# Optimization experiments

Hardware: AMD Instinct MI355X
Metric: run time of the kernel (lower is better)

The kernel has to match this reference:

```python
import jax, jax.numpy as jnp
import numpy as np

# KernelNorm2d config (matches init_kwargs)
KH, KW = 2, 2          # kernel_size
SH, SW = 2, 2          # stride
PAD = (0, 0, 0, 0)     # (left, right, top, bottom) as in F.pad on last two dims
EPS = 1e-5

B, C, H, W = 16, 64, 256, 256


def setup_inputs() -> dict:
    key = jax.random.key(0)
    x = jax.random.normal(key, (B, C, H, W), dtype=jnp.float32)
    return {"x": x}


def _kernel_norm2d(x):
    left, right, top, bottom = PAD
    xp = jnp.pad(x, ((0, 0), (0, 0), (top, bottom), (left, right)))
    b, c, hp, wp = xp.shape
    nH = (hp - KH) // SH + 1
    nW = (wp - KW) // SW + 1
    # Gather window pixels: output pixel (i*KH+a, j*KW+b) <- padded (i*SH+a, j*SW+b).
    rows = (jnp.arange(nH)[:, None] * SH + jnp.arange(KH)[None, :]).reshape(-1)
    cols = (jnp.arange(nW)[:, None] * SW + jnp.arange(KW)[None, :]).reshape(-1)
    g = xp[:, :, rows, :][:, :, :, cols]              # [B, C, nH*KH, nW*KW]
    gr = g.reshape(b, c, nH, KH, nW, KW)
    # Per-window mean/var over (C, KH, KW); biased var (unbiased=False).
    mu = jnp.mean(gr, axis=(1, 3, 5), keepdims=True)  # [B,1,nH,1,nW,1]
    m2 = jnp.mean(gr * gr, axis=(1, 3, 5), keepdims=True)
    var = m2 - mu * mu
    out = (gr - mu) / jnp.sqrt(var + EPS)
    return out.reshape(b, c, nH * KH, nW * KW)


def reference(x):
    return _kernel_norm2d(x)
```

## Files before the change

kernel.cpp:

```cpp
#include <hip/hip_runtime.h>


#define CC 64
#define HH 256
#define WW 256

__global__ __launch_bounds__(256)
void knorm2d_kernel(const float* __restrict__ x, float* __restrict__ out) {
    const int t   = threadIdx.x;
    const int blk = blockIdx.x;
    const int b   = blk >> 9;
    const int rem = blk & 511;
    const int i   = rem >> 2;
    const int cc  = rem & 3;
    const int vq  = t & 15;

    const size_t base = (size_t)b * (CC * HH * WW) + (size_t)(2 * i) * WW
                      + (size_t)(64 * cc + 4 * vq);

    float4 data[8];
    float sum[2] = {0.f, 0.f};
    float ssq[2] = {0.f, 0.f};

    #pragma unroll
    for (int k = 0; k < 8; ++k) {
        const int idx = k * 256 + t;
        const int seg = idx >> 4;
        const int c   = seg >> 1;
        const int hoff= seg & 1;
        const size_t off = base + (size_t)c * (HH * WW) + (size_t)hoff * WW;
        const float4 v = *reinterpret_cast<const float4*>(x + off);
        data[k] = v;
        sum[0] += v.x + v.y;   ssq[0] += v.x * v.x + v.y * v.y;
        sum[1] += v.z + v.w;   ssq[1] += v.z * v.z + v.w * v.w;
    }

    #pragma unroll
    for (int q = 0; q < 2; ++q) {
        sum[q] += __shfl_xor(sum[q], 16);
        ssq[q] += __shfl_xor(ssq[q], 16);
        sum[q] += __shfl_xor(sum[q], 32);
        ssq[q] += __shfl_xor(ssq[q], 32);
    }

    __shared__ float part[4][16][4];
    __shared__ float stats[32][2];

    const int wave = t >> 6;
    const int lid  = t & 63;
    if (lid < 16) {
        part[wave][lid][0] = sum[0];
        part[wave][lid][1] = ssq[0];
        part[wave][lid][2] = sum[1];
        part[wave][lid][3] = ssq[1];
    }
    __syncthreads();

    if (t < 32) {
        const int v = t >> 1;
        const int q = t & 1;
        float s = 0.f, s2 = 0.f;
        #pragma unroll
        for (int w = 0; w < 4; ++w) {
            s  += part[w][v][2 * q];
            s2 += part[w][v][2 * q + 1];
        }
        const float mu  = s  * (1.0f / 256.0f);
        const float var = s2 * (1.0f / 256.0f) - mu * mu;
        stats[t][0] = mu;
        stats[t][1] = rsqrtf(var + 1e-5f);
    }
    __syncthreads();

    const float mu0 = stats[2 * vq][0],     rs0 = stats[2 * vq][1];
    const float mu1 = stats[2 * vq + 1][0], rs1 = stats[2 * vq + 1][1];

    #pragma unroll
    for (int k = 0; k < 8; ++k) {
        const int idx = k * 256 + t;
        const int seg = idx >> 4;
        const int c   = seg >> 1;
        const int hoff= seg & 1;
        const size_t off = base + (size_t)c * (HH * WW) + (size_t)hoff * WW;
        float4 v = data[k];
        float4 o;
        o.x = (v.x - mu0) * rs0;
        o.y = (v.y - mu0) * rs0;
        o.z = (v.z - mu1) * rs1;
        o.w = (v.w - mu1) * rs1;
        *reinterpret_cast<float4*>(out + off) = o;
    }
}

extern "C" void kernel_launch(void* const* d_in, const int* in_sizes, int n_in,
                              void* d_out, int out_size, void* d_ws, size_t ws_size,
                              hipStream_t stream) {
    const float* x = (const float*)d_in[0];
    float* out     = (float*)d_out;
    knorm2d_kernel<<<dim3(8192), dim3(256), 0, stream>>>(x, out);
}
```

Baseline: 436.6 us.

## Use 1024-thread blocks covering full row pairs with nontemporal output stores

```diff
diff --git a/kernel.cpp b/kernel.cpp
--- a/kernel.cpp
+++ b/kernel.cpp
@@ -5,65 +5,52 @@
 #define HH 256
 #define WW 256
 
-__global__ __launch_bounds__(256)
+typedef float floatx4 __attribute__((ext_vector_type(4)));
+
+__global__ __launch_bounds__(1024)
 void knorm2d_kernel(const float* __restrict__ x, float* __restrict__ out) {
-    const int t   = threadIdx.x;
-    const int blk = blockIdx.x;
-    const int b   = blk >> 9;
-    const int rem = blk & 511;
-    const int i   = rem >> 2;
-    const int cc  = rem & 3;
-    const int vq  = t & 15;
+    const int t    = threadIdx.x;
+    const int b    = blockIdx.x >> 7;
+    const int i    = blockIdx.x & 127;
+    const int wave = t >> 6;
+    const int l    = t & 63;
+    const int h    = wave & 1;
+    const int w2   = wave >> 1;
 
-    const size_t base = (size_t)b * (CC * HH * WW) + (size_t)(2 * i) * WW
-                      + (size_t)(64 * cc + 4 * vq);
+    const size_t base = (size_t)b * (CC * HH * WW)
+                      + (size_t)w2 * (HH * WW)
+                      + (size_t)(2 * i + h) * WW
+                      + (size_t)(4 * l);
 
-    float4 data[8];
-    float sum[2] = {0.f, 0.f};
-    float ssq[2] = {0.f, 0.f};
+    floatx4 data[8];
+    float sum0 = 0.f, sum1 = 0.f, ssq0 = 0.f, ssq1 = 0.f;
 
     #pragma unroll
     for (int k = 0; k < 8; ++k) {
-        const int idx = k * 256 + t;
-        const int seg = idx >> 4;
-        const int c   = seg >> 1;
-        const int hoff= seg & 1;
-        const size_t off = base + (size_t)c * (HH * WW) + (size_t)hoff * WW;
-        const float4 v = *reinterpret_cast<const float4*>(x + off);
+        const size_t off = base + (size_t)k * (8 * HH * WW);
+        const floatx4 v = *reinterpret_cast<const floatx4*>(x + off);
         data[k] = v;
-        sum[0] += v.x + v.y;   ssq[0] += v.x * v.x + v.y * v.y;
-        sum[1] += v.z + v.w;   ssq[1] += v.z * v.z + v.w * v.w;
+        sum0 += v.x + v.y;   ssq0 += v.x * v.x + v.y * v.y;
+        sum1 += v.z + v.w;   ssq1 += v.z * v.z + v.w * v.w;
     }
 
-    #pragma unroll
-    for (int q = 0; q < 2; ++q) {
-        sum[q] += __shfl_xor(sum[q], 16);
-        ssq[q] += __shfl_xor(ssq[q], 16);
-        sum[q] += __shfl_xor(sum[q], 32);
-        ssq[q] += __shfl_xor(ssq[q], 32);
-    }
+    __shared__ float part[16][64][4];
+    __shared__ float stats[128][2];
 
-    __shared__ float part[4][16][4];
-    __shared__ float stats[32][2];
-
-    const int wave = t >> 6;
-    const int lid  = t & 63;
-    if (lid < 16) {
-        part[wave][lid][0] = sum[0];
-        part[wave][lid][1] = ssq[0];
-        part[wave][lid][2] = sum[1];
-        part[wave][lid][3] = ssq[1];
-    }
+    part[wave][l][0] = sum0;
+    part[wave][l][1] = ssq0;
+    part[wave][l][2] = sum1;
+    part[wave][l][3] = ssq1;
     __syncthreads();
 
-    if (t < 32) {
-        const int v = t >> 1;
-        const int q = t & 1;
+    if (t < 128) {
+        const int lw = t >> 1;
+        const int q  = t & 1;
         float s = 0.f, s2 = 0.f;
         #pragma unroll
-        for (int w = 0; w < 4; ++w) {
-            s  += part[w][v][2 * q];
-            s2 += part[w][v][2 * q + 1];
+        for (int w = 0; w < 16; ++w) {
+            s  += part[w][lw][2 * q];
+            s2 += part[w][lw][2 * q + 1];
         }
         const float mu  = s  * (1.0f / 256.0f);
         const float var = s2 * (1.0f / 256.0f) - mu * mu;
@@ -72,23 +59,19 @@
     }
     __syncthreads();
 
-    const float mu0 = stats[2 * vq][0],     rs0 = stats[2 * vq][1];
-    const float mu1 = stats[2 * vq + 1][0], rs1 = stats[2 * vq + 1][1];
+    const float mu0 = stats[2 * l][0],     rs0 = stats[2 * l][1];
+    const float mu1 = stats[2 * l + 1][0], rs1 = stats[2 * l + 1][1];
 
     #pragma unroll
     for (int k = 0; k < 8; ++k) {
-        const int idx = k * 256 + t;
-        const int seg = idx >> 4;
-        const int c   = seg >> 1;
-        const int hoff= seg & 1;
-        const size_t off = base + (size_t)c * (HH * WW) + (size_t)hoff * WW;
-        float4 v = data[k];
-        float4 o;
+        const size_t off = base + (size_t)k * (8 * HH * WW);
+        const floatx4 v = data[k];
+        floatx4 o;
         o.x = (v.x - mu0) * rs0;
         o.y = (v.y - mu0) * rs0;
         o.z = (v.z - mu1) * rs1;
         o.w = (v.w - mu1) * rs1;
-        *reinterpret_cast<float4*>(out + off) = o;
+        __builtin_nontemporal_store(o, reinterpret_cast<floatx4*>(out + off));
     }
 }
 
@@ -97,5 +80,5 @@
                               hipStream_t stream) {
     const float* x = (const float*)d_in[0];
     float* out     = (float*)d_out;
-    knorm2d_kernel<<<dim3(8192), dim3(256), 0, stream>>>(x, out);
+    knorm2d_kernel<<<dim3(2048), dim3(1024), 0, stream>>>(x, out);
 }
```

After: 444.1 us. No clear change (+1.7%).
